# Kernel tuning notes

Measured on AMD Instinct MI355X. Metric: run time of the kernel, lower is better.

The kernel has to match this reference:

```python
import jax, jax.numpy as jnp
import numpy as np

B = 2097152  # batch
H = 2        # GRU hidden size


def _gru_cell(x, h, w_ih, w_hh, b_ih, b_hh):
    # torch.nn.GRUCell math. w_ih: [3H, I], w_hh: [3H, H]
    gi = x @ w_ih.T + b_ih  # [B, 3H]
    gh = h @ w_hh.T + b_hh  # [B, 3H]
    i_r, i_z, i_n = jnp.split(gi, 3, axis=-1)
    h_r, h_z, h_n = jnp.split(gh, 3, axis=-1)
    r = jax.nn.sigmoid(i_r + h_r)
    z = jax.nn.sigmoid(i_z + h_z)
    n = jnp.tanh(i_n + r * h_n)
    return (1.0 - z) * n + z * h


def setup_inputs() -> dict:
    key = jax.random.key(0)
    ks = jax.random.split(key, 14)
    f32 = jnp.float32
    inp = {
        "x": jax.random.normal(ks[0], (B, 18), dtype=f32),
        # r_up: GRUCell(2, 2)
        "w_ih_up": 0.3 * jax.random.normal(ks[1], (3 * H, 2), dtype=f32),
        "w_hh_up": 0.3 * jax.random.normal(ks[2], (3 * H, H), dtype=f32),
        "b_ih_up": 0.1 * jax.random.normal(ks[3], (3 * H,), dtype=f32),
        "b_hh_up": 0.1 * jax.random.normal(ks[4], (3 * H,), dtype=f32),
        # fc_obs: Linear(6, 2)
        "w_obs": 0.3 * jax.random.normal(ks[5], (2, 6), dtype=f32),
        "b_obs": 0.1 * jax.random.normal(ks[6], (2,), dtype=f32),
        # r_down: GRUCell(2, 2)
        "w_ih_dn": 0.3 * jax.random.normal(ks[7], (3 * H, 2), dtype=f32),
        "w_hh_dn": 0.3 * jax.random.normal(ks[8], (3 * H, H), dtype=f32),
        "b_ih_dn": 0.1 * jax.random.normal(ks[9], (3 * H,), dtype=f32),
        "b_hh_dn": 0.1 * jax.random.normal(ks[10], (3 * H,), dtype=f32),
        # fc_out: Linear(2, 1)
        "w_out": 0.3 * jax.random.normal(ks[11], (1, H), dtype=f32),
        "b_out": 0.1 * jax.random.normal(ks[12], (1,), dtype=f32),
    }
    return inp


def reference(x, w_ih_up, w_hh_up, b_ih_up, b_hh_up, w_obs, b_obs,
              w_ih_dn, w_hh_dn, b_ih_dn, b_hh_dn, w_out, b_out):
    obs = x[:, :4]            # [B, 4]
    j = x[:, 4:11]            # [B, 7]
    jd = x[:, 11:]            # [B, 7]
    jcat = jnp.stack([j, jd], axis=1)  # [B, 2, 7]

    # upward recurrence over the 7 joints, reversed order
    h = jnp.zeros((x.shape[0], H), dtype=x.dtype)
    h_up = []
    for i in reversed(range(7)):
        h = _gru_cell(jcat[:, :, i], h, w_ih_up, w_hh_up, b_ih_up, b_hh_up)
        h_up.append(h)

    # fuse observation into the hidden state
    h = jnp.concatenate([obs, h], axis=1) @ w_obs.T + b_obs  # [B, 2]

    # downward recurrence, emitting one action per joint
    acts = []
    for i in range(7):
        h = _gru_cell(h_up[i], h, w_ih_dn, w_hh_dn, b_ih_dn, b_hh_dn)
        acts.append(h @ w_out.T + b_out)  # [B, 1]
    return jnp.concatenate(acts, axis=1)  # [B, 7]
```

## Files before the change

### kernel.cpp

```cpp
#include <hip/hip_runtime.h>


using v2f = __attribute__((ext_vector_type(2))) float;

__device__ __forceinline__ float fexp2(float x) { return __builtin_amdgcn_exp2f(x); }
__device__ __forceinline__ float frcp(float x)  { return __builtin_amdgcn_rcpf(x); }

struct Cell {
    v2f wr0, wr1, ur0, ur1, br;
    v2f wz0, wz1, uz0, uz1, bz;
    v2f wn0, wn1, bni;
    v2f un0, un1, bnh;
};

__global__ void prep_kernel(
    const float* __restrict__ w_ih_up, const float* __restrict__ w_hh_up,
    const float* __restrict__ b_ih_up, const float* __restrict__ b_hh_up,
    const float* __restrict__ w_obs,   const float* __restrict__ b_obs,
    const float* __restrict__ w_ih_dn, const float* __restrict__ w_hh_dn,
    const float* __restrict__ b_ih_dn, const float* __restrict__ b_hh_dn,
    const float* __restrict__ w_out,   const float* __restrict__ b_out,
    float* __restrict__ ws)
{
    if (threadIdx.x != 0 || blockIdx.x != 0) return;
    const float s1 = -1.4426950408889634f;
    const float s2 =  2.8853900817779268f;
    #pragma unroll
    for (int c = 0; c < 2; ++c) {
        const float* wi = c ? w_ih_dn : w_ih_up;
        const float* wh = c ? w_hh_dn : w_hh_up;
        const float* bi = c ? b_ih_dn : b_ih_up;
        const float* bh = c ? b_hh_dn : b_hh_up;
        float* o = ws + c * 64;
        o[0] = s1*wi[0]; o[1] = s1*wi[2];  o[2] = s1*wi[1]; o[3] = s1*wi[3];
        o[4] = s1*wh[0]; o[5] = s1*wh[2];  o[6] = s1*wh[1]; o[7] = s1*wh[3];
        o[8] = s1*(bi[0]+bh[0]); o[9] = s1*(bi[1]+bh[1]);
        o[10] = s1*wi[4]; o[11] = s1*wi[6]; o[12] = s1*wi[5]; o[13] = s1*wi[7];
        o[14] = s1*wh[4]; o[15] = s1*wh[6]; o[16] = s1*wh[5]; o[17] = s1*wh[7];
        o[18] = s1*(bi[2]+bh[2]); o[19] = s1*(bi[3]+bh[3]);
        o[20] = s2*wi[8]; o[21] = s2*wi[10]; o[22] = s2*wi[9]; o[23] = s2*wi[11];
        o[24] = s2*bi[4]; o[25] = s2*bi[5];
        o[26] = s2*wh[8]; o[27] = s2*wh[10]; o[28] = s2*wh[9]; o[29] = s2*wh[11];
        o[30] = s2*bh[4]; o[31] = s2*bh[5];
    }
    #pragma unroll
    for (int i = 0; i < 12; ++i) ws[128 + i] = w_obs[i];
    ws[140] = b_obs[0]; ws[141] = b_obs[1];
    ws[142] = w_out[0]; ws[143] = w_out[1];
    ws[144] = b_out[0];
}

__device__ __forceinline__ void gru(const Cell& c, float x0, float x1, v2f& h) {
    v2f gr = c.br + c.wr0 * x0 + c.wr1 * x1 + c.ur0 * h.x + c.ur1 * h.y;
    v2f gz = c.bz + c.wz0 * x0 + c.wz1 * x1 + c.uz0 * h.x + c.uz1 * h.y;
    v2f dr = (v2f){1.0f + fexp2(gr.x), 1.0f + fexp2(gr.y)};
    v2f dz = (v2f){1.0f + fexp2(gz.x), 1.0f + fexp2(gz.y)};
    float invr = frcp(dr.x * dr.y);
    v2f r = invr * (v2f){dr.y, dr.x};
    v2f gi = c.bni + c.wn0 * x0 + c.wn1 * x1;
    v2f gh = c.bnh + c.un0 * h.x + c.un1 * h.y;
    v2f a  = gi + r * gh;
    v2f da = (v2f){1.0f + fexp2(a.x), 1.0f + fexp2(a.y)};
    float m = -2.0f * frcp(da.x * da.y);
    v2f n = (v2f){fmaf(m, da.y, 1.0f), fmaf(m, da.x, 1.0f)};
    float invz = frcp(dz.x * dz.y);
    v2f z = invz * (v2f){dz.y, dz.x};
    h = n + z * (h - n);
}

__device__ __forceinline__ void row_chain(
    const Cell& up, const Cell& dn, const float* __restrict__ W,
    const float* row, float acts[7])
{
    v2f h = (v2f){0.0f, 0.0f};
    v2f hu[7];
    #pragma unroll
    for (int k = 0; k < 7; ++k) {
        const int i = 6 - k;
        gru(up, row[4 + i], row[11 + i], h);
        hu[k] = h;
    }
    {
        v2f t = (v2f){W[140], W[141]};
        #pragma unroll
        for (int c = 0; c < 4; ++c)
            t += (v2f){W[128 + c], W[134 + c]} * row[c];
        t += (v2f){W[132], W[138]} * h.x;
        t += (v2f){W[133], W[139]} * h.y;
        h = t;
    }
    const float wo0 = W[142], wo1 = W[143], bo = W[144];
    #pragma unroll
    for (int k = 0; k < 7; ++k) {
        gru(dn, hu[k].x, hu[k].y, h);
        acts[k] = fmaf(wo0, h.x, fmaf(wo1, h.y, bo));
    }
}

__global__ __launch_bounds__(256) void recpolicy_kernel(
    const float* __restrict__ x, const float* __restrict__ W,
    float* __restrict__ out, int n)
{
    __shared__ float lds[4608];
    const int tid  = threadIdx.x;
    const int wid  = tid >> 6;
    const int lane = tid & 63;
    float* wlds = lds + wid * 1152;

    const Cell up = *reinterpret_cast<const Cell*>(W);
    const Cell dn = *reinterpret_cast<const Cell*>(W + 64);

    const int NT = n >> 6;
    const int NW = gridDim.x << 2;
    const int gw = (blockIdx.x << 2) | wid;

    const float4* xs = reinterpret_cast<const float4*>(x);

    int t = gw;
    if (t < NT) {
        float4 nx0, nx1, nx2, nx3, nx4;
        {
            size_t b = (size_t)t * 288;
            nx0 = xs[b + lane];       nx1 = xs[b + 64 + lane];
            nx2 = xs[b + 128 + lane]; nx3 = xs[b + 192 + lane];
            if (lane < 32) nx4 = xs[b + 256 + lane];
        }
        while (true) {
            {
                float4* d = reinterpret_cast<float4*>(wlds);
                d[lane] = nx0;       d[lane + 64]  = nx1;
                d[lane + 128] = nx2; d[lane + 192] = nx3;
                if (lane < 32) d[lane + 256] = nx4;
            }
            const int tn = t + NW;
            if (tn < NT) {
                size_t b = (size_t)tn * 288;
                nx0 = xs[b + lane];       nx1 = xs[b + 64 + lane];
                nx2 = xs[b + 128 + lane]; nx3 = xs[b + 192 + lane];
                if (lane < 32) nx4 = xs[b + 256 + lane];
            }

            const float* row = wlds + lane * 18;
            float acts[7];
            row_chain(up, dn, W, row, acts);

            #pragma unroll
            for (int k = 0; k < 7; ++k) wlds[lane * 7 + k] = acts[k];
            {
                const float4* so = reinterpret_cast<const float4*>(wlds);
                float4* dsto = reinterpret_cast<float4*>(out) + (size_t)t * 112;
                dsto[lane] = so[lane];
                if (lane < 48) dsto[lane + 64] = so[lane + 64];
            }

            if (tn >= NT) break;
            t = tn;
        }
    }

    const int tail0 = NT << 6;
    if (gw == 0 && tail0 < n) {
        const int rg = tail0 + lane;
        if (rg < n) {
            float rowl[18];
            #pragma unroll
            for (int i = 0; i < 18; ++i) rowl[i] = x[(size_t)rg * 18 + i];
            float acts[7];
            row_chain(up, dn, W, rowl, acts);
            #pragma unroll
            for (int k = 0; k < 7; ++k) out[(size_t)rg * 7 + k] = acts[k];
        }
    }
}

extern "C" void kernel_launch(void* const* d_in, const int* in_sizes, int n_in,
                              void* d_out, int out_size, void* d_ws, size_t ws_size,
                              hipStream_t stream) {
    const float* x       = (const float*)d_in[0];
    const float* w_ih_up = (const float*)d_in[1];
    const float* w_hh_up = (const float*)d_in[2];
    const float* b_ih_up = (const float*)d_in[3];
    const float* b_hh_up = (const float*)d_in[4];
    const float* w_obs   = (const float*)d_in[5];
    const float* b_obs   = (const float*)d_in[6];
    const float* w_ih_dn = (const float*)d_in[7];
    const float* w_hh_dn = (const float*)d_in[8];
    const float* b_ih_dn = (const float*)d_in[9];
    const float* b_hh_dn = (const float*)d_in[10];
    const float* w_out   = (const float*)d_in[11];
    const float* b_out   = (const float*)d_in[12];
    float* out = (float*)d_out;
    float* ws  = (float*)d_ws;

    prep_kernel<<<1, 64, 0, stream>>>(
        w_ih_up, w_hh_up, b_ih_up, b_hh_up, w_obs, b_obs,
        w_ih_dn, w_hh_dn, b_ih_dn, b_hh_dn, w_out, b_out, ws);

    const int n = in_sizes[0] / 18;
    recpolicy_kernel<<<2048, 256, 0, stream>>>(x, ws, out, n);
}
```

Before: 53.63 us.

## Load input tiles directly into LDS with async global_load_lds prefetch

Input tiles are now fetched with global_load_lds, which writes straight into LDS without staging through registers. Each row is copied into registers, and only then is the next tile's load issued into the same buffer, so the prefetch overlaps the GRU compute. Outputs get their own LDS region so the staging write cannot clash with the in-flight input load. The grid also shrinks from 2048 to 1536 blocks, and the larger LDS footprint may lower occupancy.

```diff
diff --git a/kernel.cpp b/kernel.cpp
--- a/kernel.cpp
+++ b/kernel.cpp
@@ -97,57 +97,71 @@
     }
 }
 
+__device__ __forceinline__ void dma_tile(const float* __restrict__ x,
+                                         size_t t, float* in_lds, int lane)
+{
+    const char* g = reinterpret_cast<const char*>(x) + t * 4608;
+    char* l = reinterpret_cast<char*>(in_lds);
+    #pragma unroll
+    for (int k = 0; k < 4; ++k) {
+        __builtin_amdgcn_global_load_lds(
+            (const __attribute__((address_space(1))) void*)(g + k * 1024 + lane * 16),
+            (__attribute__((address_space(3))) void*)(l + k * 1024), 16, 0, 0);
+    }
+    #pragma unroll
+    for (int c = 0; c < 2; ++c) {
+        __builtin_amdgcn_global_load_lds(
+            (const __attribute__((address_space(1))) void*)(g + 4096 + c * 256 + lane * 4),
+            (__attribute__((address_space(3))) void*)(l + 4096 + c * 256), 4, 0, 0);
+    }
+}
+
 __global__ __launch_bounds__(256) void recpolicy_kernel(
     const float* __restrict__ x, const float* __restrict__ W,
     float* __restrict__ out, int n)
 {
-    __shared__ float lds[4608];
+    __shared__ float lds[4 * 1600];
     const int tid  = threadIdx.x;
     const int wid  = tid >> 6;
     const int lane = tid & 63;
-    float* wlds = lds + wid * 1152;
+    float* inb  = lds + wid * 1600;
+    float* outb = inb + 1152;
 
     const Cell up = *reinterpret_cast<const Cell*>(W);
     const Cell dn = *reinterpret_cast<const Cell*>(W + 64);
 
     const int NT = n >> 6;
     const int NW = gridDim.x << 2;
-    const int gw = (blockIdx.x << 2) | wid;
-
-    const float4* xs = reinterpret_cast<const float4*>(x);
-
-    int t = gw;
+    int t = (blockIdx.x << 2) | wid;
+
     if (t < NT) {
-        float4 nx0, nx1, nx2, nx3, nx4;
-        {
-            size_t b = (size_t)t * 288;
-            nx0 = xs[b + lane];       nx1 = xs[b + 64 + lane];
-            nx2 = xs[b + 128 + lane]; nx3 = xs[b + 192 + lane];
-            if (lane < 32) nx4 = xs[b + 256 + lane];
-        }
+        dma_tile(x, (size_t)t, inb, lane);
         while (true) {
+            asm volatile("s_waitcnt vmcnt(0)" ::: "memory");
+            __builtin_amdgcn_sched_barrier(0);
+
+            float rowv[18];
             {
-                float4* d = reinterpret_cast<float4*>(wlds);
-                d[lane] = nx0;       d[lane + 64]  = nx1;
-                d[lane + 128] = nx2; d[lane + 192] = nx3;
-                if (lane < 32) d[lane + 256] = nx4;
+                const float2* rp = reinterpret_cast<const float2*>(inb + lane * 18);
+                #pragma unroll
+                for (int i = 0; i < 9; ++i) {
+                    float2 v = rp[i];
+                    rowv[2 * i] = v.x; rowv[2 * i + 1] = v.y;
+                }
             }
+            asm volatile("s_waitcnt lgkmcnt(0)" ::: "memory");
+            __builtin_amdgcn_sched_barrier(0);
+
             const int tn = t + NW;
-            if (tn < NT) {
-                size_t b = (size_t)tn * 288;
-                nx0 = xs[b + lane];       nx1 = xs[b + 64 + lane];
-                nx2 = xs[b + 128 + lane]; nx3 = xs[b + 192 + lane];
-                if (lane < 32) nx4 = xs[b + 256 + lane];
-            }
-
-            const float* row = wlds + lane * 18;
+            if (tn < NT) dma_tile(x, (size_t)tn, inb, lane);
+
             float acts[7];
-            row_chain(up, dn, W, row, acts);
+            row_chain(up, dn, W, rowv, acts);
 
             #pragma unroll
-            for (int k = 0; k < 7; ++k) wlds[lane * 7 + k] = acts[k];
+            for (int k = 0; k < 7; ++k) outb[lane * 7 + k] = acts[k];
             {
-                const float4* so = reinterpret_cast<const float4*>(wlds);
+                const float4* so = reinterpret_cast<const float4*>(outb);
                 float4* dsto = reinterpret_cast<float4*>(out) + (size_t)t * 112;
                 dsto[lane] = so[lane];
                 if (lane < 48) dsto[lane + 64] = so[lane + 64];
@@ -159,7 +173,7 @@
     }
 
     const int tail0 = NT << 6;
-    if (gw == 0 && tail0 < n) {
+    if (blockIdx.x == 0 && wid == 0 && tail0 < n) {
         const int rg = tail0 + lane;
         if (rg < n) {
             float rowl[18];
@@ -197,5 +211,5 @@
         w_ih_dn, w_hh_dn, b_ih_dn, b_hh_dn, w_out, b_out, ws);
 
     const int n = in_sizes[0] / 18;
-    recpolicy_kernel<<<2048, 256, 0, stream>>>(x, ws, out, n);
-}
+    recpolicy_kernel<<<1536, 256, 0, stream>>>(x, ws, out, n);
+}
```

Result: slower. 54.73 us (+2.1%).
